# Kernel optimization log

Measured on AMD Instinct MI355X. Metric: run time of the kernel, lower is better.

## Reference

```python
import jax, jax.numpy as jnp
import numpy as np

H = 16  # num_heads

def setup_inputs() -> dict:
    key = jax.random.key(0)
    ks = jax.random.split(key, 6)
    B, T, C, S = 2, 2048, 1024, 2048
    return {
        "q": jax.random.normal(ks[0], (B, T, C), jnp.float32),
        "k_xl": jax.random.normal(ks[1], (B, S, C), jnp.float32),
        "v_xl": jax.random.normal(ks[2], (B, S, C), jnp.float32),
        "W_qkv": jax.random.normal(ks[3], (3 * C, C), jnp.float32) * (1.0 / np.sqrt(C)),
        "W_proj": jax.random.normal(ks[4], (C, C), jnp.float32) * (1.0 / np.sqrt(C)),
        "pos_emb": jax.random.normal(ks[5], (S, C), jnp.float32),
        "is_causal": 0,
    }

def reference(q, k_xl, v_xl, W_qkv, W_proj, pos_emb, is_causal):
    B, T, C = q.shape
    hd = C // H
    # self_attention: W_qkv(q).split(d_model, -1)
    qkv = jnp.einsum('btc,dc->btd', q, W_qkv)  # [B,T,3C]
    qn, kn, vn = jnp.split(qkv, 3, axis=-1)
    # XL cache gets positional embedding added before use
    kx = k_xl + pos_emb[None, :, :]            # [B,S,C]
    vx = v_xl

    def to_heads(x):
        b, s, c = x.shape
        return x.reshape(b, s, H, hd).transpose(0, 2, 1, 3)  # [B,H,s,hd]

    qh = to_heads(qn)
    kcat = jnp.concatenate([to_heads(kx), to_heads(kn)], axis=2)  # [B,H,S+T,hd]
    vcat = jnp.concatenate([to_heads(vx), to_heads(vn)], axis=2)
    scale = 1.0 / jnp.sqrt(jnp.asarray(hd, qh.dtype))
    scores = jnp.einsum('bhtd,bhsd->bhts', qh, kcat) * scale  # [B,H,T,S+T]
    attn = jax.nn.softmax(scores, axis=-1)
    y = jnp.einsum('bhts,bhsd->bhtd', attn, vcat)  # [B,H,T,hd]
    y = y.transpose(0, 2, 1, 3).reshape(B, T, C)
    return jnp.einsum('btc,dc->btd', y, W_proj)
```

## Files before the change

kernel.cpp:

```cpp
#include <hip/hip_runtime.h>

typedef unsigned short u16;
typedef unsigned int u32;
typedef u16 u16x4 __attribute__((ext_vector_type(4)));
typedef u16 u16x8 __attribute__((ext_vector_type(8)));
typedef __bf16 bf16x8 __attribute__((ext_vector_type(8)));
typedef float f32x4 __attribute__((ext_vector_type(4)));
typedef float f32x16 __attribute__((ext_vector_type(16)));

static __device__ __forceinline__ u16 f2bf(float f) {
  union { float f; u32 u; } x; x.f = f;
  u32 r = x.u + 0x7fffu + ((x.u >> 16) & 1u);
  return (u16)(r >> 16);
}
static __device__ __forceinline__ u32 packbf(float a, float b) {
  union { u32 u; __bf16 h[2]; } x; x.h[0] = (__bf16)a; x.h[1] = (__bf16)b; return x.u;
}
static __device__ __forceinline__ void pl32swap(u32& a, u32& b) {
  asm volatile("v_permlane32_swap_b32 %0, %1" : "+v"(a), "+v"(b));
}
static __device__ __forceinline__ void gload16(const void* g, void* l) {
  __builtin_amdgcn_global_load_lds((const __attribute__((address_space(1))) unsigned int*)g,
                                   (__attribute__((address_space(3))) unsigned int*)l, 16, 0, 0);
}

__global__ __launch_bounds__(256) void cvt_all(const float* __restrict__ q, const float* __restrict__ wqkv_f,
                                               const float* __restrict__ wproj_f, u16* __restrict__ qbf,
                                               u16* __restrict__ wqkv, u16* __restrict__ wproj, float sc) {
  int i = blockIdx.x * 256 + threadIdx.x;
  const float* src;
  u16* dst;
  int j;
  float s = 1.0f;
  if (i < 1048576) { src = q; dst = qbf; j = i; }
  else if (i < 1835008) { j = i - 1048576; src = wqkv_f; dst = wqkv; if (j < 262144) s = sc; }
  else { j = i - 1835008; src = wproj_f; dst = wproj; }
  float4 v = reinterpret_cast<const float4*>(src)[j];
  u16x4 o; o[0] = f2bf(v.x * s); o[1] = f2bf(v.y * s); o[2] = f2bf(v.z * s); o[3] = f2bf(v.w * s);
  reinterpret_cast<u16x4*>(dst)[j] = o;
}

template <int OUT_BF16>
__global__ __launch_bounds__(256, 2) void gemm_bt2(const u16* __restrict__ A, const u16* __restrict__ B,
                                                   void* __restrict__ Cout, int M, int N, int K) {
  __shared__ alignas(128) u16 As[8192];
  __shared__ alignas(128) u16 Bs[8192];
  const int tid = threadIdx.x;
  const int m0 = blockIdx.y * 128, n0 = blockIdx.x * 128;
  const int wid = tid >> 6, lane = tid & 63;
  const int lm = lane & 15, lg = lane >> 4;
  const int wm = (wid >> 1) * 64, wn = (wid & 1) * 64;
  int srow[4], scol[4];
#pragma unroll
  for (int i = 0; i < 4; i++) {
    int li = tid + i * 256;
    srow[i] = li >> 3;
    scol[i] = ((li & 7) ^ (srow[i] & 7)) * 8;
  }
  f32x4 acc[4][4] = {};
  for (int k0 = 0; k0 < K; k0 += 64) {
    __syncthreads();
#pragma unroll
    for (int i = 0; i < 4; i++) {
      gload16(&A[(size_t)(m0 + srow[i]) * K + k0 + scol[i]], &As[(size_t)(i * 256 + wid * 64) * 8]);
      gload16(&B[(size_t)(n0 + srow[i]) * K + k0 + scol[i]], &Bs[(size_t)(i * 256 + wid * 64) * 8]);
    }
    __syncthreads();
#pragma unroll
    for (int ks = 0; ks < 2; ks++) {
      bf16x8 af[4], bfr[4];
#pragma unroll
      for (int mi = 0; mi < 4; mi++) {
        int row = wm + mi * 16 + lm;
        af[mi] = *(const bf16x8*)&As[row * 64 + (((ks * 4 + lg) ^ (row & 7)) << 3)];
      }
#pragma unroll
      for (int ni = 0; ni < 4; ni++) {
        int row = wn + ni * 16 + lm;
        bfr[ni] = *(const bf16x8*)&Bs[row * 64 + (((ks * 4 + lg) ^ (row & 7)) << 3)];
      }
#pragma unroll
      for (int mi = 0; mi < 4; mi++)
#pragma unroll
        for (int ni = 0; ni < 4; ni++)
          acc[mi][ni] = __builtin_amdgcn_mfma_f32_16x16x32_bf16(af[mi], bfr[ni], acc[mi][ni], 0, 0, 0);
    }
  }
#pragma unroll
  for (int mi = 0; mi < 4; mi++)
#pragma unroll
    for (int ni = 0; ni < 4; ni++)
#pragma unroll
      for (int r = 0; r < 4; r++) {
        int row = m0 + wm + mi * 16 + lg * 4 + r;
        int col = n0 + wn + ni * 16 + lm;
        if (OUT_BF16) ((u16*)Cout)[(size_t)row * N + col] = f2bf(acc[mi][ni][r]);
        else          ((float*)Cout)[(size_t)row * N + col] = acc[mi][ni][r];
      }
}

__global__ __launch_bounds__(256) void build_kxl(const float* __restrict__ k_xl, const float* __restrict__ pos,
                                                 u16* __restrict__ khxl) {
  int idx = blockIdx.x * 256 + threadIdx.x;
  int d8 = idx & 7;
  int s = (idx >> 3) & 2047;
  int bh = idx >> 14;
  int b = bh >> 4, h = bh & 15;
  size_t src = ((size_t)(b * 2048 + s)) * 1024 + h * 64 + d8 * 8;
  size_t ps = ((size_t)s) * 1024 + h * 64 + d8 * 8;
  float4 a0 = *(const float4*)&k_xl[src];
  float4 a1 = *(const float4*)&k_xl[src + 4];
  float4 p0 = *(const float4*)&pos[ps];
  float4 p1 = *(const float4*)&pos[ps + 4];
  u16x8 o;
  o[0] = f2bf(a0.x + p0.x); o[1] = f2bf(a0.y + p0.y); o[2] = f2bf(a0.z + p0.z); o[3] = f2bf(a0.w + p0.w);
  o[4] = f2bf(a1.x + p1.x); o[5] = f2bf(a1.y + p1.y); o[6] = f2bf(a1.z + p1.z); o[7] = f2bf(a1.w + p1.w);
  *(u16x8*)&khxl[((size_t)bh * 2048 + s) * 64 + d8 * 8] = o;
}

__global__ __launch_bounds__(256) void build_vt(const float* __restrict__ v_xl, const u16* __restrict__ qkvb,
                                                u16* __restrict__ Vt) {
  __shared__ u16 tile[64][72];
  const int bh = blockIdx.y, b = bh >> 4, h = bh & 15;
  const int s0 = blockIdx.x * 64;
  const int tid = threadIdx.x;
  {
    int sl = tid >> 2;
    int dseg = (tid & 3) * 16;
    if (s0 < 2048) {
      const float* src = v_xl + ((size_t)(b * 2048 + s0 + sl)) * 1024 + h * 64 + dseg;
#pragma unroll
      for (int j = 0; j < 16; j += 4) {
        float4 v = *(const float4*)&src[j];
        tile[sl][dseg + j] = f2bf(v.x);
        tile[sl][dseg + j + 1] = f2bf(v.y);
        tile[sl][dseg + j + 2] = f2bf(v.z);
        tile[sl][dseg + j + 3] = f2bf(v.w);
      }
    } else {
      const u16* src = qkvb + ((size_t)(b * 2048 + s0 - 2048 + sl)) * 3072 + 2048 + h * 64 + dseg;
      *(u16x8*)&tile[sl][dseg] = *(const u16x8*)&src[0];
      *(u16x8*)&tile[sl][dseg + 8] = *(const u16x8*)&src[8];
    }
  }
  __syncthreads();
  {
    int d = tid >> 2;
    int sseg = (tid & 3) * 16;
    u16* dst = Vt + ((size_t)bh * 64 + d) * 4096 + s0 + sseg;
    u16x8 o0, o1;
#pragma unroll
    for (int j = 0; j < 8; j++) { o0[j] = tile[sseg + j][d]; o1[j] = tile[sseg + 8 + j][d]; }
    *(u16x8*)&dst[0] = o0;
    *(u16x8*)&dst[8] = o1;
  }
}

__global__ __launch_bounds__(256, 2) void attn_fwd4(const u16* __restrict__ qkvb, const u16* __restrict__ khxl,
                                                    const u16* __restrict__ vt, u16* __restrict__ Y) {
  const int T = 2048;
  __shared__ alignas(128) u16 KsF[2][4096];
  __shared__ alignas(128) u16 VsF[2][4096];
  const int bh = blockIdx.y;
  const int q0 = blockIdx.x * 128;
  const int tid = threadIdx.x, wid = tid >> 6, lane = tid & 63;
  const int l31 = lane & 31, hi = lane >> 5;
  const int sw = l31 & 7;
  const int b = bh >> 4, h = bh & 15;
  const int q = q0 + wid * 32 + l31;
  const u16* Qp = qkvb + (size_t)(b * T + q) * 3072 + h * 64;
  bf16x8 qf[4];
#pragma unroll
  for (int c = 0; c < 4; c++) qf[c] = *(const bf16x8*)&Qp[c * 16 + hi * 8];
  const u16* kxl_p[2];
  const u16* knew_p[2];
  const u16* v_p[2];
  int dsto[2];
#pragma unroll
  for (int i = 0; i < 2; i++) {
    int li = tid + i * 256;
    int srow = li >> 3, scol = ((li & 7) ^ (srow & 7)) * 8;
    kxl_p[i] = khxl + (size_t)bh * 2048 * 64 + (size_t)srow * 64 + scol;
    knew_p[i] = qkvb + (size_t)(b * T + srow) * 3072 + 1024 + h * 64 + scol;
    v_p[i] = vt + ((size_t)bh * 64 + srow) * 4096 + scol;
    dsto[i] = (i * 256 + wid * 64) * 8;
  }
  f32x16 accA = {0.0f}, accB = {0.0f};
  float lrun = 0.0f;
#pragma unroll
  for (int i = 0; i < 2; i++) {
    gload16(kxl_p[i], &KsF[0][dsto[i]]);
    gload16(v_p[i], &VsF[0][dsto[i]]);
  }
  int cur = 0;
  for (int t = 0; t < 64; ++t) {
    __syncthreads();
    if (t + 1 < 64) {
      const int nt = t + 1;
#pragma unroll
      for (int i = 0; i < 2; i++) {
        const u16* ksrc = (nt < 32) ? kxl_p[i] + (size_t)nt * 4096
                                    : knew_p[i] + (size_t)(nt - 32) * 196608;
        gload16(ksrc, &KsF[cur ^ 1][dsto[i]]);
        gload16(v_p[i] + nt * 64, &VsF[cur ^ 1][dsto[i]]);
      }
    }
    const u16* Ksb = KsF[cur];
    const u16* Vsb = VsF[cur];
#pragma unroll
    for (int half = 0; half < 2; half++) {
      const int krow = half * 32 + l31;
      f32x16 s = {0.0f};
      __builtin_amdgcn_s_setprio(1);
#pragma unroll
      for (int c = 0; c < 4; c++) {
        int cg = 2 * c + hi;
        bf16x8 kf = *(const bf16x8*)&Ksb[krow * 64 + ((cg ^ sw) << 3)];
        s = __builtin_amdgcn_mfma_f32_32x32x16_bf16(kf, qf[c], s, 0, 0, 0);
      }
      __builtin_amdgcn_s_setprio(0);
#pragma unroll
      for (int r = 0; r < 16; r++) s[r] = __builtin_amdgcn_exp2f(s[r]);
      float r0 = ((s[0] + s[1]) + (s[2] + s[3])) + ((s[4] + s[5]) + (s[6] + s[7]));
      float r1 = ((s[8] + s[9]) + (s[10] + s[11])) + ((s[12] + s[13]) + (s[14] + s[15]));
      lrun += r0 + r1;
      u32 w[4][2];
#pragma unroll
      for (int g = 0; g < 4; g++) {
        w[g][0] = packbf(s[4 * g + 0], s[4 * g + 1]);
        w[g][1] = packbf(s[4 * g + 2], s[4 * g + 3]);
      }
      __builtin_amdgcn_s_setprio(1);
#pragma unroll
      for (int m2 = 0; m2 < 2; m2++) {
        int m = half * 2 + m2;
        u32 W0 = w[2 * m2][0], W2 = w[2 * m2 + 1][0];
        pl32swap(W0, W2);
        u32 W1 = w[2 * m2][1], W3 = w[2 * m2 + 1][1];
        pl32swap(W1, W3);
        union { u32 u[4]; bf16x8 v; } pf;
        pf.u[0] = W0; pf.u[1] = W1; pf.u[2] = W2; pf.u[3] = W3;
        int cg = 2 * m + hi;
        bf16x8 v0 = *(const bf16x8*)&Vsb[l31 * 64 + ((cg ^ sw) << 3)];
        bf16x8 v1 = *(const bf16x8*)&Vsb[(32 + l31) * 64 + ((cg ^ sw) << 3)];
        accA = __builtin_amdgcn_mfma_f32_32x32x16_bf16(v0, pf.v, accA, 0, 0, 0);
        accB = __builtin_amdgcn_mfma_f32_32x32x16_bf16(v1, pf.v, accB, 0, 0, 0);
      }
      __builtin_amdgcn_s_setprio(0);
    }
    cur ^= 1;
  }
  float lt = lrun + __shfl_xor(lrun, 32);
  float inv = 1.0f / lt;
  __syncthreads();
  u16* Ts = (u16*)KsF + wid * 2048;
#pragma unroll
  for (int dt = 0; dt < 2; dt++)
#pragma unroll
    for (int r2 = 0; r2 < 4; r2++) {
      u16x4 o;
#pragma unroll
      for (int e = 0; e < 4; e++) {
        float v = dt ? accB[4 * r2 + e] : accA[4 * r2 + e];
        o[e] = f2bf(v * inv);
      }
      int dbase = dt * 32 + r2 * 8 + hi * 4;
      int byteoff = l31 * 128 + ((dbase * 2) ^ (sw << 4));
      *(u16x4*)((char*)Ts + byteoff) = o;
    }
  __syncthreads();
#pragma unroll
  for (int p = 0; p < 4; p++) {
    int row = p * 8 + (lane >> 3);
    int c16 = lane & 7;
    u16x8 v = *(const u16x8*)((const char*)Ts + row * 128 + ((c16 << 4) ^ ((row & 7) << 4)));
    *(u16x8*)&Y[((size_t)(b * T + q0 + wid * 32 + row)) * 1024 + h * 64 + c16 * 8] = v;
  }
}

extern "C" void kernel_launch(void* const* d_in, const int* in_sizes, int n_in,
                              void* d_out, int out_size, void* d_ws, size_t ws_size,
                              hipStream_t stream) {
  const float* q = (const float*)d_in[0];
  const float* k_xl = (const float*)d_in[1];
  const float* v_xl = (const float*)d_in[2];
  const float* W_qkv = (const float*)d_in[3];
  const float* W_proj = (const float*)d_in[4];
  const float* pos = (const float*)d_in[5];

  u16* wqkv = (u16*)d_ws;
  u16* wproj = wqkv + (size_t)3072 * 1024;
  u16* qbf = wproj + (size_t)1024 * 1024;
  u16* qkvb = qbf + (size_t)4096 * 1024;
  u16* khxl = qkvb + (size_t)4096 * 3072;
  u16* vt = khxl + (size_t)4 * 1024 * 1024;
  u16* ybf = vt + (size_t)8 * 1024 * 1024;

  const float SC = 0.125f * 1.4426950408889634f;

  cvt_all<<<8192, 256, 0, stream>>>(q, W_qkv, W_proj, qbf, wqkv, wproj, SC);

  gemm_bt2<1><<<dim3(24, 32), 256, 0, stream>>>(qbf, wqkv, qkvb, 4096, 3072, 1024);

  build_kxl<<<2048, 256, 0, stream>>>(k_xl, pos, khxl);
  build_vt<<<dim3(64, 32), 256, 0, stream>>>(v_xl, qkvb, vt);

  attn_fwd4<<<dim3(16, 32), 256, 0, stream>>>(qkvb, khxl, vt, ybf);

  gemm_bt2<0><<<dim3(8, 32), 256, 0, stream>>>(ybf, wproj, d_out, 4096, 1024, 1024);
}
```

Baseline: 184.6 us.

## Split KV across wave pairs in attention to halve query tile and double grid

Attention blocks now cover 64 queries instead of 128, with the four waves arranged as two query tiles by two key halves within each 64-key tile. The two key-half partial accumulators and row sums are combined through shared memory before normalization and store. The grid doubles and launch bounds allow four blocks per CU to improve occupancy and latency hiding. In exchange, K/V tiles are loaded twice as often per query and there is an extra cross-wave reduction step.

Measured after the change: 180.3 us. 2.3% less time.

```diff
diff --git a/kernel.cpp b/kernel.cpp
--- a/kernel.cpp
+++ b/kernel.cpp
@@ -156,18 +156,19 @@
   }
 }
 
-__global__ __launch_bounds__(256, 2) void attn_fwd4(const u16* __restrict__ qkvb, const u16* __restrict__ khxl,
+__global__ __launch_bounds__(256, 4) void attn_fwd5(const u16* __restrict__ qkvb, const u16* __restrict__ khxl,
                                                     const u16* __restrict__ vt, u16* __restrict__ Y) {
   const int T = 2048;
   __shared__ alignas(128) u16 KsF[2][4096];
   __shared__ alignas(128) u16 VsF[2][4096];
   const int bh = blockIdx.y;
-  const int q0 = blockIdx.x * 128;
+  const int q0 = blockIdx.x * 64;
   const int tid = threadIdx.x, wid = tid >> 6, lane = tid & 63;
+  const int qt = wid & 1, ks = wid >> 1;
   const int l31 = lane & 31, hi = lane >> 5;
   const int sw = l31 & 7;
   const int b = bh >> 4, h = bh & 15;
-  const int q = q0 + wid * 32 + l31;
+  const int q = q0 + qt * 32 + l31;
   const u16* Qp = qkvb + (size_t)(b * T + q) * 3072 + h * 64;
   bf16x8 qf[4];
 #pragma unroll
@@ -193,6 +194,7 @@
     gload16(v_p[i], &VsF[0][dsto[i]]);
   }
   int cur = 0;
+  const int krow = ks * 32 + l31;
   for (int t = 0; t < 64; ++t) {
     __syncthreads();
     if (t + 1 < 64) {
@@ -207,74 +209,83 @@
     }
     const u16* Ksb = KsF[cur];
     const u16* Vsb = VsF[cur];
-#pragma unroll
-    for (int half = 0; half < 2; half++) {
-      const int krow = half * 32 + l31;
-      f32x16 s = {0.0f};
-      __builtin_amdgcn_s_setprio(1);
-#pragma unroll
-      for (int c = 0; c < 4; c++) {
-        int cg = 2 * c + hi;
-        bf16x8 kf = *(const bf16x8*)&Ksb[krow * 64 + ((cg ^ sw) << 3)];
-        s = __builtin_amdgcn_mfma_f32_32x32x16_bf16(kf, qf[c], s, 0, 0, 0);
-      }
-      __builtin_amdgcn_s_setprio(0);
-#pragma unroll
-      for (int r = 0; r < 16; r++) s[r] = __builtin_amdgcn_exp2f(s[r]);
-      float r0 = ((s[0] + s[1]) + (s[2] + s[3])) + ((s[4] + s[5]) + (s[6] + s[7]));
-      float r1 = ((s[8] + s[9]) + (s[10] + s[11])) + ((s[12] + s[13]) + (s[14] + s[15]));
-      lrun += r0 + r1;
-      u32 w[4][2];
-#pragma unroll
-      for (int g = 0; g < 4; g++) {
-        w[g][0] = packbf(s[4 * g + 0], s[4 * g + 1]);
-        w[g][1] = packbf(s[4 * g + 2], s[4 * g + 3]);
-      }
-      __builtin_amdgcn_s_setprio(1);
-#pragma unroll
-      for (int m2 = 0; m2 < 2; m2++) {
-        int m = half * 2 + m2;
-        u32 W0 = w[2 * m2][0], W2 = w[2 * m2 + 1][0];
-        pl32swap(W0, W2);
-        u32 W1 = w[2 * m2][1], W3 = w[2 * m2 + 1][1];
-        pl32swap(W1, W3);
-        union { u32 u[4]; bf16x8 v; } pf;
-        pf.u[0] = W0; pf.u[1] = W1; pf.u[2] = W2; pf.u[3] = W3;
-        int cg = 2 * m + hi;
-        bf16x8 v0 = *(const bf16x8*)&Vsb[l31 * 64 + ((cg ^ sw) << 3)];
-        bf16x8 v1 = *(const bf16x8*)&Vsb[(32 + l31) * 64 + ((cg ^ sw) << 3)];
-        accA = __builtin_amdgcn_mfma_f32_32x32x16_bf16(v0, pf.v, accA, 0, 0, 0);
-        accB = __builtin_amdgcn_mfma_f32_32x32x16_bf16(v1, pf.v, accB, 0, 0, 0);
-      }
-      __builtin_amdgcn_s_setprio(0);
-    }
+    f32x16 s = {0.0f};
+    __builtin_amdgcn_s_setprio(1);
+#pragma unroll
+    for (int c = 0; c < 4; c++) {
+      int cg = 2 * c + hi;
+      bf16x8 kf = *(const bf16x8*)&Ksb[krow * 64 + ((cg ^ sw) << 3)];
+      s = __builtin_amdgcn_mfma_f32_32x32x16_bf16(kf, qf[c], s, 0, 0, 0);
+    }
+    __builtin_amdgcn_s_setprio(0);
+#pragma unroll
+    for (int r = 0; r < 16; r++) s[r] = __builtin_amdgcn_exp2f(s[r]);
+    float r0 = ((s[0] + s[1]) + (s[2] + s[3])) + ((s[4] + s[5]) + (s[6] + s[7]));
+    float r1 = ((s[8] + s[9]) + (s[10] + s[11])) + ((s[12] + s[13]) + (s[14] + s[15]));
+    lrun += r0 + r1;
+    u32 w[4][2];
+#pragma unroll
+    for (int g = 0; g < 4; g++) {
+      w[g][0] = packbf(s[4 * g + 0], s[4 * g + 1]);
+      w[g][1] = packbf(s[4 * g + 2], s[4 * g + 3]);
+    }
+    __builtin_amdgcn_s_setprio(1);
+#pragma unroll
+    for (int m2 = 0; m2 < 2; m2++) {
+      int m = ks * 2 + m2;
+      u32 W0 = w[2 * m2][0], W2 = w[2 * m2 + 1][0];
+      pl32swap(W0, W2);
+      u32 W1 = w[2 * m2][1], W3 = w[2 * m2 + 1][1];
+      pl32swap(W1, W3);
+      union { u32 u[4]; bf16x8 v; } pf;
+      pf.u[0] = W0; pf.u[1] = W1; pf.u[2] = W2; pf.u[3] = W3;
+      int cg = 2 * m + hi;
+      bf16x8 v0 = *(const bf16x8*)&Vsb[l31 * 64 + ((cg ^ sw) << 3)];
+      bf16x8 v1 = *(const bf16x8*)&Vsb[(32 + l31) * 64 + ((cg ^ sw) << 3)];
+      accA = __builtin_amdgcn_mfma_f32_32x32x16_bf16(v0, pf.v, accA, 0, 0, 0);
+      accB = __builtin_amdgcn_mfma_f32_32x32x16_bf16(v1, pf.v, accB, 0, 0, 0);
+    }
+    __builtin_amdgcn_s_setprio(0);
     cur ^= 1;
   }
   float lt = lrun + __shfl_xor(lrun, 32);
-  float inv = 1.0f / lt;
   __syncthreads();
-  u16* Ts = (u16*)KsF + wid * 2048;
-#pragma unroll
-  for (int dt = 0; dt < 2; dt++)
-#pragma unroll
-    for (int r2 = 0; r2 < 4; r2++) {
-      u16x4 o;
-#pragma unroll
-      for (int e = 0; e < 4; e++) {
-        float v = dt ? accB[4 * r2 + e] : accA[4 * r2 + e];
-        o[e] = f2bf(v * inv);
-      }
-      int dbase = dt * 32 + r2 * 8 + hi * 4;
-      int byteoff = l31 * 128 + ((dbase * 2) ^ (sw << 4));
-      *(u16x4*)((char*)Ts + byteoff) = o;
-    }
+  float* CB = (float*)KsF;
+  if (ks) {
+    float* p = CB + (size_t)(qt * 64 + lane) * 33;
+#pragma unroll
+    for (int r = 0; r < 16; r++) { p[r] = accA[r]; p[16 + r] = accB[r]; }
+    p[32] = lt;
+  }
   __syncthreads();
-#pragma unroll
-  for (int p = 0; p < 4; p++) {
-    int row = p * 8 + (lane >> 3);
-    int c16 = lane & 7;
-    u16x8 v = *(const u16x8*)((const char*)Ts + row * 128 + ((c16 << 4) ^ ((row & 7) << 4)));
-    *(u16x8*)&Y[((size_t)(b * T + q0 + wid * 32 + row)) * 1024 + h * 64 + c16 * 8] = v;
+  if (!ks) {
+    const float* p = CB + (size_t)(qt * 64 + lane) * 33;
+#pragma unroll
+    for (int r = 0; r < 16; r++) { accA[r] += p[r]; accB[r] += p[16 + r]; }
+    lt += p[32];
+    float inv = 1.0f / lt;
+    u16* Ts = (u16*)((char*)VsF + 1024 + qt * 4096);
+#pragma unroll
+    for (int dt = 0; dt < 2; dt++)
+#pragma unroll
+      for (int r2 = 0; r2 < 4; r2++) {
+        u16x4 o;
+#pragma unroll
+        for (int e = 0; e < 4; e++) {
+          float v = dt ? accB[4 * r2 + e] : accA[4 * r2 + e];
+          o[e] = f2bf(v * inv);
+        }
+        int dbase = dt * 32 + r2 * 8 + hi * 4;
+        int byteoff = l31 * 128 + ((dbase * 2) ^ (sw << 4));
+        *(u16x4*)((char*)Ts + byteoff) = o;
+      }
+#pragma unroll
+    for (int p4 = 0; p4 < 4; p4++) {
+      int row = p4 * 8 + (lane >> 3);
+      int c16 = lane & 7;
+      u16x8 v = *(const u16x8*)((const char*)Ts + row * 128 + ((c16 << 4) ^ ((row & 7) << 4)));
+      *(u16x8*)&Y[((size_t)(b * T + q0 + qt * 32 + row)) * 1024 + h * 64 + c16 * 8] = v;
+    }
   }
 }
 
@@ -305,7 +316,7 @@
   build_kxl<<<2048, 256, 0, stream>>>(k_xl, pos, khxl);
   build_vt<<<dim3(64, 32), 256, 0, stream>>>(v_xl, qkvb, vt);
 
-  attn_fwd4<<<dim3(16, 32), 256, 0, stream>>>(qkvb, khxl, vt, ybf);
+  attn_fwd5<<<dim3(32, 32), 256, 0, stream>>>(qkvb, khxl, vt, ybf);
 
   gemm_bt2<0><<<dim3(8, 32), 256, 0, stream>>>(ybf, wproj, d_out, 4096, 1024, 1024);
 }
```
